# Performance work log

Measured on AMD Instinct MI355X. Metric: run time of the kernel, lower is better.

Reference implementation:

```python
import jax, jax.numpy as jnp
import numpy as np

B, S, F, D, U, DS = 128, 64, 32, 128, 128, 128  # batch, seq, features, feat_dim, units, static_dim
DIN = S * F * D + DS  # grn_concat input dim
EPS = 1e-3  # keras LayerNormalization default epsilon


def _ln(x, gamma, beta):
    m = jnp.mean(x, axis=-1, keepdims=True)
    v = jnp.mean(jnp.square(x - m), axis=-1, keepdims=True)
    return (x - m) * jax.lax.rsqrt(v + EPS) * gamma + beta


def setup_inputs() -> dict:
    key = jax.random.key(0)
    ks = iter(jax.random.split(key, 32))
    p = lambda *shape: jax.random.normal(next(ks), shape, dtype=jnp.float32) * 0.02
    inp = {
        "inputs": jax.random.normal(next(ks), (B, S, F * D), dtype=jnp.float32),
        "static_input": jax.random.normal(next(ks), (B, DS), dtype=jnp.float32),
        # grn_concat (input dim DIN != U -> project path active)
        "cWe": p(DIN, U), "cbe": jnp.zeros((U,), jnp.float32),
        "cWl": p(U, U), "cbl": jnp.zeros((U,), jnp.float32),
        "cWgl": p(U, U), "cbgl": jnp.zeros((U,), jnp.float32),
        "cWgs": p(U, U), "cbgs": jnp.zeros((U,), jnp.float32),
        "cgamma": jnp.ones((U,), jnp.float32), "cbeta": jnp.zeros((U,), jnp.float32),
        "cWp": p(DIN, U), "cbp": jnp.zeros((U,), jnp.float32),
        # softmax Dense: units -> num_features
        "Ws": p(U, F), "bs": jnp.zeros((F,), jnp.float32),
        # per-feature GRNs, stacked over feature axis (feat_dim == units -> no project)
        "fWe": p(F, D, U), "fbe": jnp.zeros((F, U), jnp.float32),
        "fWl": p(F, U, U), "fbl": jnp.zeros((F, U), jnp.float32),
        "fWgl": p(F, U, U), "fbgl": jnp.zeros((F, U), jnp.float32),
        "fWgs": p(F, U, U), "fbgs": jnp.zeros((F, U), jnp.float32),
        "fgamma": jnp.ones((F, U), jnp.float32), "fbeta": jnp.zeros((F, U), jnp.float32),
    }
    return inp


def reference(inputs, static_input, cWe, cbe, cWl, cbl, cWgl, cbgl, cWgs, cbgs,
              cgamma, cbeta, cWp, cbp, Ws, bs, fWe, fbe, fWl, fbl, fWgl, fbgl,
              fWgs, fbgs, fgamma, fbeta):
    b = inputs.shape[0]
    # --- selection weights: flatten + concat static, grn_concat, softmax dense ---
    v = jnp.concatenate([inputs.reshape(b, -1), static_input], axis=-1)  # [B, DIN]
    h = jax.nn.elu(v @ cWe + cbe)
    h = h @ cWl + cbl
    res = v @ cWp + cbp  # project (DIN != U)
    g = (h @ cWgl + cbgl) * jax.nn.sigmoid(h @ cWgs + cbgs)  # GLU
    y = _ln(res + g, cgamma, cbeta)  # [B, U]
    w = jax.nn.softmax(y @ Ws + bs, axis=-1)  # [B, F]
    # --- per-feature GRNs, batched over feature axis ---
    x = inputs.reshape(b, S, F, D)  # tf.split along axis 2
    h = jax.nn.elu(jnp.einsum('bsfd,fdu->bsfu', x, fWe) + fbe)
    h = jnp.einsum('bsfu,fuv->bsfv', h, fWl) + fbl
    g = (jnp.einsum('bsfu,fuv->bsfv', h, fWgl) + fbgl) * \
        jax.nn.sigmoid(jnp.einsum('bsfu,fuv->bsfv', h, fWgs) + fbgs)
    xg = _ln(x + g, fgamma, fbeta)  # [B, S, F, U]
    # --- softmax-weighted combine (v repeated over seq, matmul transpose_a) ---
    out = jnp.einsum('bf,bsfu->bsu', w, xg)  # [B, S, U]
    return out
```

## Files before the change

### kernel.cpp

```cpp
#include <hip/hip_runtime.h>


typedef unsigned short u16;
typedef __attribute__((ext_vector_type(4))) u16 u16x4;
typedef __attribute__((ext_vector_type(8))) u16 u16x8;
typedef __attribute__((ext_vector_type(8))) __bf16 bf16x8;
typedef __attribute__((ext_vector_type(4))) float f32x4;

__device__ __forceinline__ u16 f2bf(float f) {
  unsigned int x = __float_as_uint(f);
  return (u16)((x + 0x7fffu + ((x >> 16) & 1u)) >> 16);
}
__device__ __forceinline__ float eluf(float x) { return x > 0.f ? x : __expf(x) - 1.f; }
__device__ __forceinline__ float sigmoidf_(float x) { return 1.f / (1.f + __expf(-x)); }

#define MFMA_BF16(a, b, c) __builtin_amdgcn_mfma_f32_16x16x32_bf16((a), (b), (c), 0, 0, 0)

__global__ __launch_bounds__(512) void k0_prep(
    const float* __restrict__ fWe, const float* __restrict__ fWl,
    const float* __restrict__ fWgl, const float* __restrict__ fWgs,
    u16* __restrict__ wT)
{
  const int b = blockIdx.x, f = b >> 2, mat = b & 3;
  const float* srcs[4] = {fWe, fWl, fWgl, fWgs};
  const float* src = srcs[mat] + (size_t)f * 16384;
  u16* dst = wT + (size_t)b * 16384;
  const int n = threadIdx.x & 127, qc = threadIdx.x >> 7;
  for (int k8 = qc * 4; k8 < qc * 4 + 4; ++k8) {
    u16x8 p;
#pragma unroll
    for (int j = 0; j < 8; ++j) p[j] = f2bf(src[(k8 * 8 + j) * 128 + n]);
    *(u16x8*)&dst[n * 128 + k8 * 8] = p;
  }
}

__global__ __launch_bounds__(1024) void k1_bigmm(
    const float* __restrict__ inp, const float* __restrict__ cWe,
    const float* __restrict__ cWp, float* __restrict__ outE, float* __restrict__ outP)
{
  __shared__ __align__(16) u16 xA[2][128][64];
  __shared__ __align__(16) u16 wE[2][128][64];
  __shared__ __align__(16) u16 wP[2][128][64];
  const int t = threadIdx.x;
  const int lane = t & 63, wv = t >> 6, quad = lane >> 4, l16 = lane & 15;
  const int mat = wv >> 3, wvm = wv & 7;
  const int arow = t >> 3, af = t & 7;
  const int aslot = (af ^ (arow & 7)) * 8;
  const int wt = t & 511, wmi = t >> 9;
  const int wn = wt & 127, wkg = wt >> 7;
  const int wphi = (wn ^ (wn >> 2)) & 7;
  const float* Wm = wmi ? cWp : cWe;

  f32x4 acc[8];
#pragma unroll
  for (int n = 0; n < 8; ++n)
#pragma unroll
    for (int r = 0; r < 4; ++r) acc[n][r] = 0.f;

  const size_t kbase = (size_t)blockIdx.x * 1024;

  float4 av0[2], av1[2];
  float wv0[16], wv1[16];

  auto load_regs = [&](int it, float4* av, float* wr) {
    const size_t kk = kbase + (size_t)it * 64;
    av[0] = *(const float4*)(inp + (size_t)arow * 262144 + kk + af * 8);
    av[1] = *(const float4*)(inp + (size_t)arow * 262144 + kk + af * 8 + 4);
#pragma unroll
    for (int j = 0; j < 16; ++j)
      wr[j] = Wm[(kk + (size_t)(wkg * 16 + j)) * 128 + wn];
  };
  auto store_lds = [&](int buf, const float4* av, const float* wr) {
    u16x8 pa;
    pa[0] = f2bf(av[0].x); pa[1] = f2bf(av[0].y);
    pa[2] = f2bf(av[0].z); pa[3] = f2bf(av[0].w);
    pa[4] = f2bf(av[1].x); pa[5] = f2bf(av[1].y);
    pa[6] = f2bf(av[1].z); pa[7] = f2bf(av[1].w);
    *(u16x8*)&xA[buf][arow][aslot] = pa;
    u16 (*Wl)[64] = wmi ? wP[buf] : wE[buf];
#pragma unroll
    for (int s = 0; s < 2; ++s) {
      u16x8 pw;
#pragma unroll
      for (int j = 0; j < 8; ++j) pw[j] = f2bf(wr[s * 8 + j]);
      *(u16x8*)&Wl[wn][((wkg * 2 + s) ^ wphi) * 8] = pw;
    }
  };

  load_regs(0, av0, wv0);
  load_regs(1, av1, wv1);
  store_lds(0, av0, wv0);

  const int m = 16 * wvm + l16;
  const int phA = l16 & 7;
  const int phB = (l16 & 7) ^ (l16 >> 2);

  for (int it = 0; it < 16; ++it) {
    const int buf = it & 1;
    asm volatile("s_waitcnt lgkmcnt(0)" ::: "memory");
    __builtin_amdgcn_s_barrier();
    if (it < 14) {
      if (buf == 0) load_regs(it + 2, av0, wv0);
      else          load_regs(it + 2, av1, wv1);
    }
    const u16 (*Xb)[64] = xA[buf];
    const u16 (*WbT)[64] = mat ? wP[buf] : wE[buf];
#pragma unroll
    for (int ks = 0; ks < 2; ++ks) {
      const int slot = ks * 4 + quad;
      const bf16x8 a = *(const bf16x8*)&Xb[m][(slot ^ phA) * 8];
#pragma unroll
      for (int nt = 0; nt < 8; ++nt) {
        const bf16x8 b = *(const bf16x8*)&WbT[nt * 16 + l16][(slot ^ phB ^ ((nt & 1) * 4)) * 8];
        acc[nt] = MFMA_BF16(a, b, acc[nt]);
      }
    }
    if (it < 15) {
      if (buf == 0) store_lds(1, av1, wv1);
      else          store_lds(0, av0, wv0);
    }
  }
  float* outp = mat ? outP : outE;
#pragma unroll
  for (int nt = 0; nt < 8; ++nt) {
    const int col = nt * 16 + l16;
#pragma unroll
    for (int r = 0; r < 4; ++r) {
      const int row = 16 * wvm + quad * 4 + r;
      atomicAdd(&outp[row * 128 + col], acc[nt][r]);
    }
  }
}

__global__ __launch_bounds__(512) void k1b_small(
    const float* __restrict__ stat,
    const float* __restrict__ cWe, const float* __restrict__ cbe,
    const float* __restrict__ cWl, const float* __restrict__ cbl,
    const float* __restrict__ cWgl, const float* __restrict__ cbgl,
    const float* __restrict__ cWgs, const float* __restrict__ cbgs,
    const float* __restrict__ cgam, const float* __restrict__ cbet,
    const float* __restrict__ cWp, const float* __restrict__ cbp,
    const float* __restrict__ Ws, const float* __restrict__ bs,
    const float* __restrict__ preE, const float* __restrict__ preP,
    float* __restrict__ wout)
{
  const int b = blockIdx.x, t = threadIdx.x;
  const int u = t & 127, dc = t >> 7;
  __shared__ float shS[128], shA[128], shB[128], par[8][132], red[4];
  if (t < 128) shS[t] = stat[b * 128 + t];
  __syncthreads();

  const float* we = cWe + (size_t)262144 * 128;
  const float* wp = cWp + (size_t)262144 * 128;
  float hp = 0.f, rp = 0.f;
  for (int d = dc * 32; d < dc * 32 + 32; ++d) {
    const float sv = shS[d];
    hp += sv * we[d * 128 + u];
    rp += sv * wp[d * 128 + u];
  }
  par[dc][u] = hp; par[4 + dc][u] = rp;
  __syncthreads();

  float rs = 0.f;
  if (t < 128) {
    const float he = preE[b * 128 + t] + cbe[t] + par[0][t] + par[1][t] + par[2][t] + par[3][t];
    rs = preP[b * 128 + t] + cbp[t] + par[4][t] + par[5][t] + par[6][t] + par[7][t];
    shA[t] = eluf(he);
  }
  __syncthreads();

  float p = 0.f;
  for (int d = dc * 32; d < dc * 32 + 32; ++d) p += shA[d] * cWl[d * 128 + u];
  par[dc][u] = p;
  __syncthreads();
  if (t < 128) shB[t] = cbl[t] + par[0][t] + par[1][t] + par[2][t] + par[3][t];
  __syncthreads();

  float gp = 0.f, sp = 0.f;
  for (int d = dc * 32; d < dc * 32 + 32; ++d) {
    const float hv = shB[d];
    gp += hv * cWgl[d * 128 + u];
    sp += hv * cWgs[d * 128 + u];
  }
  par[dc][u] = gp; par[4 + dc][u] = sp;
  __syncthreads();

  float z = 0.f;
  if (t < 128) {
    const float gl = cbgl[t] + par[0][t] + par[1][t] + par[2][t] + par[3][t];
    const float gs = cbgs[t] + par[4][t] + par[5][t] + par[6][t] + par[7][t];
    z = rs + gl * sigmoidf_(gs);
  }
  float s = z, q = z * z;
#pragma unroll
  for (int off = 32; off >= 1; off >>= 1) { s += __shfl_xor(s, off); q += __shfl_xor(q, off); }
  if ((t & 63) == 0 && t < 128) { red[(t >> 6) * 2] = s; red[(t >> 6) * 2 + 1] = q; }
  __syncthreads();
  if (t < 128) {
    const float S = red[0] + red[2], Q = red[1] + red[3];
    const float mean = S * (1.f / 128.f);
    const float var = Q * (1.f / 128.f) - mean * mean;
    const float rstd = rsqrtf(var + 1e-3f);
    shA[t] = (z - mean) * rstd * cgam[t] + cbet[t];
  }
  __syncthreads();
  if (t < 32) {
    float sj = bs[t];
    for (int uu = 0; uu < 128; ++uu) sj += shA[uu] * Ws[uu * 32 + t];
    float m = sj;
#pragma unroll
    for (int off = 16; off >= 1; off >>= 1) m = fmaxf(m, __shfl_xor(m, off));
    const float e = __expf(sj - m);
    float se = e;
#pragma unroll
    for (int off = 16; off >= 1; off >>= 1) se += __shfl_xor(se, off);
    wout[b * 32 + t] = e / se;
  }
}

__device__ __forceinline__ void mm_half(const u16 A[][136], const u16 WT[][72],
                                        int wv, int quad, int l16, int kh, f32x4 acc[8])
{
#pragma unroll
  for (int ks = 0; ks < 2; ++ks) {
    const int kol = ks * 32 + quad * 8;
    const bf16x8 a = *(const bf16x8*)&A[16 * wv + l16][kh + kol];
#pragma unroll
    for (int nt = 0; nt < 8; ++nt) {
      const bf16x8 b = *(const bf16x8*)&WT[nt * 16 + l16][kol];
      acc[nt] = MFMA_BF16(a, b, acc[nt]);
    }
  }
}

__global__ __launch_bounds__(256) void k2_grn(
    const float* __restrict__ inp, const u16* __restrict__ wT,
    const float* __restrict__ fbe, const float* __restrict__ fbl,
    const float* __restrict__ fbgl, const float* __restrict__ fbgs,
    const float* __restrict__ fgam, const float* __restrict__ fbet,
    const float* __restrict__ wsel, float* __restrict__ out)
{
  __shared__ __align__(16) u16 xA[64][136];
  __shared__ __align__(16) u16 hA[64][136];
  __shared__ __align__(16) u16 WT[2][128][72];
  const int t = threadIdx.x;
  const int lane = t & 63, wv = t >> 6, quad = lane >> 4, l16 = lane & 15;
  const int bb = blockIdx.x & 127, fg = blockIdx.x >> 7;

  f32x4 acc[8], glr[8], racc[8];
#pragma unroll
  for (int n = 0; n < 8; ++n)
#pragma unroll
    for (int r = 0; r < 4; ++r) racc[n][r] = 0.f;

#define ZERO_ACC() do { _Pragma("unroll") \
  for (int n_ = 0; n_ < 8; ++n_) { acc[n_][0]=0.f; acc[n_][1]=0.f; acc[n_][2]=0.f; acc[n_][3]=0.f; } } while (0)

  u16x8 wreg[4];
  auto wt_load = [&](const u16* src) {
#pragma unroll
    for (int i = 0; i < 4; ++i) {
      const int u = t + i * 256;
      wreg[i] = *(const u16x8*)(src + (u >> 3) * 128 + (u & 7) * 8);
    }
  };
  auto wt_write = [&](int nb) {
#pragma unroll
    for (int i = 0; i < 4; ++i) {
      const int u = t + i * 256;
      *(u16x8*)&WT[nb][u >> 3][(u & 7) * 8] = wreg[i];
    }
  };

  for (int fi = 0; fi < 8; ++fi) {
    const int f = fg * 8 + fi;
    const float wb = wsel[bb * 32 + f];
    const u16* wf = wT + (size_t)f * 65536;

    __syncthreads();
#pragma unroll
    for (int i = 0; i < 8; ++i) {
      const int u = t + i * 256;
      const int row = u >> 5, fo = u & 31;
      const float4 v = *(const float4*)(inp + (size_t)(bb * 64 + row) * 4096 + f * 128 + fo * 4);
      u16x4 p; p[0] = f2bf(v.x); p[1] = f2bf(v.y); p[2] = f2bf(v.z); p[3] = f2bf(v.w);
      *(u16x4*)&xA[row][fo * 4] = p;
    }
    wt_load(wf);
    wt_write(0);
    __syncthreads();

    wt_load(wf + 64);
    ZERO_ACC();
    mm_half(xA, WT[0], wv, quad, l16, 0, acc);
    wt_write(1);
    __syncthreads();
    wt_load(wf + 16384);
    mm_half(xA, WT[1], wv, quad, l16, 64, acc);
#pragma unroll
    for (int nt = 0; nt < 8; ++nt) {
      const int col = nt * 16 + l16;
      const float bv = fbe[f * 128 + col];
#pragma unroll
      for (int r = 0; r < 4; ++r)
        hA[16 * wv + quad * 4 + r][col] = f2bf(eluf(acc[nt][r] + bv));
    }
    wt_write(0);
    __syncthreads();

    wt_load(wf + 16384 + 64);
    ZERO_ACC();
    mm_half(hA, WT[0], wv, quad, l16, 0, acc);
    wt_write(1);
    __syncthreads();
    wt_load(wf + 2 * 16384);
    mm_half(hA, WT[1], wv, quad, l16, 64, acc);
#pragma unroll
    for (int nt = 0; nt < 8; ++nt) {
      const int col = nt * 16 + l16;
      const float bv = fbl[f * 128 + col];
#pragma unroll
      for (int r = 0; r < 4; ++r)
        hA[16 * wv + quad * 4 + r][col] = f2bf(acc[nt][r] + bv);
    }
    wt_write(0);
    __syncthreads();

    wt_load(wf + 2 * 16384 + 64);
    ZERO_ACC();
    mm_half(hA, WT[0], wv, quad, l16, 0, acc);
    wt_write(1);
    __syncthreads();
    wt_load(wf + 3 * 16384);
    mm_half(hA, WT[1], wv, quad, l16, 64, acc);
#pragma unroll
    for (int nt = 0; nt < 8; ++nt) {
      const float bv = fbgl[f * 128 + nt * 16 + l16];
#pragma unroll
      for (int r = 0; r < 4; ++r) glr[nt][r] = acc[nt][r] + bv;
    }
    wt_write(0);
    __syncthreads();

    wt_load(wf + 3 * 16384 + 64);
    ZERO_ACC();
    mm_half(hA, WT[0], wv, quad, l16, 0, acc);
    wt_write(1);
    __syncthreads();
    mm_half(hA, WT[1], wv, quad, l16, 64, acc);

#pragma unroll
    for (int nt = 0; nt < 8; ++nt) {
      const int col = nt * 16 + l16;
      const float bv = fbgs[f * 128 + col];
#pragma unroll
      for (int r = 0; r < 4; ++r) {
        const float g = glr[nt][r] * sigmoidf_(acc[nt][r] + bv);
        const float x = __uint_as_float(((unsigned int)xA[16 * wv + quad * 4 + r][col]) << 16);
        acc[nt][r] = x + g;
      }
    }
    float sm[4], sq[4];
#pragma unroll
    for (int r = 0; r < 4; ++r) {
      float s = 0.f, q = 0.f;
#pragma unroll
      for (int nt = 0; nt < 8; ++nt) { const float zz = acc[nt][r]; s += zz; q += zz * zz; }
      sm[r] = s; sq[r] = q;
    }
#pragma unroll
    for (int off = 1; off <= 8; off <<= 1)
#pragma unroll
      for (int r = 0; r < 4; ++r) { sm[r] += __shfl_xor(sm[r], off); sq[r] += __shfl_xor(sq[r], off); }
#pragma unroll
    for (int r = 0; r < 4; ++r) {
      const float mean = sm[r] * (1.f / 128.f);
      const float var = sq[r] * (1.f / 128.f) - mean * mean;
      const float rstd = rsqrtf(var + 1e-3f);
      sm[r] = mean; sq[r] = rstd;
    }
#pragma unroll
    for (int nt = 0; nt < 8; ++nt) {
      const int col = nt * 16 + l16;
      const float gam = fgam[f * 128 + col];
      const float bet = fbet[f * 128 + col];
#pragma unroll
      for (int r = 0; r < 4; ++r) {
        const float xg = (acc[nt][r] - sm[r]) * sq[r] * gam + bet;
        racc[nt][r] += wb * xg;
      }
    }
  }

#pragma unroll
  for (int nt = 0; nt < 8; ++nt) {
    const int col = nt * 16 + l16;
#pragma unroll
    for (int r = 0; r < 4; ++r) {
      const int grow = bb * 64 + 16 * wv + quad * 4 + r;
      atomicAdd(&out[(size_t)grow * 128 + col], racc[nt][r]);
    }
  }
#undef ZERO_ACC
}

extern "C" void kernel_launch(void* const* d_in, const int* in_sizes, int n_in,
                              void* d_out, int out_size, void* d_ws, size_t ws_size,
                              hipStream_t stream)
{
  const float* inp    = (const float*)d_in[0];
  const float* stat   = (const float*)d_in[1];
  const float* cWe    = (const float*)d_in[2];
  const float* cbe    = (const float*)d_in[3];
  const float* cWl    = (const float*)d_in[4];
  const float* cbl    = (const float*)d_in[5];
  const float* cWgl   = (const float*)d_in[6];
  const float* cbgl   = (const float*)d_in[7];
  const float* cWgs   = (const float*)d_in[8];
  const float* cbgs   = (const float*)d_in[9];
  const float* cgamma = (const float*)d_in[10];
  const float* cbeta  = (const float*)d_in[11];
  const float* cWp    = (const float*)d_in[12];
  const float* cbp    = (const float*)d_in[13];
  const float* Ws     = (const float*)d_in[14];
  const float* bs     = (const float*)d_in[15];
  const float* fWe    = (const float*)d_in[16];
  const float* fbe    = (const float*)d_in[17];
  const float* fWl    = (const float*)d_in[18];
  const float* fbl    = (const float*)d_in[19];
  const float* fWgl   = (const float*)d_in[20];
  const float* fbgl   = (const float*)d_in[21];
  const float* fWgs   = (const float*)d_in[22];
  const float* fbgs   = (const float*)d_in[23];
  const float* fgam   = (const float*)d_in[24];
  const float* fbet   = (const float*)d_in[25];

  float* ws_he  = (float*)d_ws;
  float* ws_res = ws_he + 16384;
  float* ws_w   = ws_res + 16384;
  u16*   ws_wT  = (u16*)(ws_w + 4096);

  hipMemsetAsync(d_ws, 0, 32768 * sizeof(float), stream);
  hipMemsetAsync(d_out, 0, (size_t)out_size * sizeof(float), stream);
  k0_prep<<<128, 512, 0, stream>>>(fWe, fWl, fWgl, fWgs, ws_wT);
  k1_bigmm<<<256, 1024, 0, stream>>>(inp, cWe, cWp, ws_he, ws_res);
  k1b_small<<<128, 512, 0, stream>>>(stat, cWe, cbe, cWl, cbl, cWgl, cbgl, cWgs, cbgs,
                                     cgamma, cbeta, cWp, cbp, Ws, bs, ws_he, ws_res, ws_w);
  k2_grn<<<512, 256, 0, stream>>>(inp, ws_wT, fbe, fbl, fbgl, fbgs,
                                  fgam, fbet, ws_w, (float*)d_out);
}
```

Measured before the change: 592.3 us.

## Read GRN weights directly from global memory and drop shared-memory staging and barriers

The per-feature GRN kernel no longer stages transposed weight tiles through a double-buffered LDS buffer. Each wave now loads its MFMA B operands straight from global memory (expected to be L2-resident) and works only on its own 16 rows, so all block-level barriers go away. The grid doubles to 1024 blocks with each handling 4 features instead of 8, the block index order is changed so blocks sharing a batch row run adjacently, and launch bounds request 4 blocks per CU. The cost is that every wave re-reads the full weights from cache instead of sharing one LDS copy, and each output element receives twice as many atomic adds.

```diff
diff --git a/kernel.cpp b/kernel.cpp
--- a/kernel.cpp
+++ b/kernel.cpp
@@ -218,22 +218,7 @@
   }
 }
 
-__device__ __forceinline__ void mm_half(const u16 A[][136], const u16 WT[][72],
-                                        int wv, int quad, int l16, int kh, f32x4 acc[8])
-{
-#pragma unroll
-  for (int ks = 0; ks < 2; ++ks) {
-    const int kol = ks * 32 + quad * 8;
-    const bf16x8 a = *(const bf16x8*)&A[16 * wv + l16][kh + kol];
-#pragma unroll
-    for (int nt = 0; nt < 8; ++nt) {
-      const bf16x8 b = *(const bf16x8*)&WT[nt * 16 + l16][kol];
-      acc[nt] = MFMA_BF16(a, b, acc[nt]);
-    }
-  }
-}
-
-__global__ __launch_bounds__(256) void k2_grn(
+__global__ __launch_bounds__(256, 4) void k2_grn(
     const float* __restrict__ inp, const u16* __restrict__ wT,
     const float* __restrict__ fbe, const float* __restrict__ fbl,
     const float* __restrict__ fbgl, const float* __restrict__ fbgs,
@@ -242,10 +227,10 @@
 {
   __shared__ __align__(16) u16 xA[64][136];
   __shared__ __align__(16) u16 hA[64][136];
-  __shared__ __align__(16) u16 WT[2][128][72];
   const int t = threadIdx.x;
   const int lane = t & 63, wv = t >> 6, quad = lane >> 4, l16 = lane & 15;
-  const int bb = blockIdx.x & 127, fg = blockIdx.x >> 7;
+  const int fg = blockIdx.x & 7, bb = blockIdx.x >> 3;
+  const int rbase = wv * 16;
 
   f32x4 acc[8], glr[8], racc[8];
 #pragma unroll
@@ -256,98 +241,67 @@
 #define ZERO_ACC() do { _Pragma("unroll") \
   for (int n_ = 0; n_ < 8; ++n_) { acc[n_][0]=0.f; acc[n_][1]=0.f; acc[n_][2]=0.f; acc[n_][3]=0.f; } } while (0)
 
-  u16x8 wreg[4];
-  auto wt_load = [&](const u16* src) {
-#pragma unroll
-    for (int i = 0; i < 4; ++i) {
-      const int u = t + i * 256;
-      wreg[i] = *(const u16x8*)(src + (u >> 3) * 128 + (u & 7) * 8);
+  auto mm_g = [&](const u16 (*A)[136], const u16* __restrict__ wg, f32x4* ac) {
+#pragma unroll
+    for (int s = 0; s < 4; ++s) {
+      const int kol = s * 32 + quad * 8;
+      const bf16x8 a = *(const bf16x8*)&A[rbase + l16][kol];
+#pragma unroll
+      for (int nt = 0; nt < 8; ++nt) {
+        const bf16x8 b = *(const bf16x8*)(wg + (size_t)(nt * 16 + l16) * 128 + kol);
+        ac[nt] = MFMA_BF16(a, b, ac[nt]);
+      }
     }
   };
-  auto wt_write = [&](int nb) {
-#pragma unroll
-    for (int i = 0; i < 4; ++i) {
-      const int u = t + i * 256;
-      *(u16x8*)&WT[nb][u >> 3][(u & 7) * 8] = wreg[i];
-    }
-  };
-
-  for (int fi = 0; fi < 8; ++fi) {
-    const int f = fg * 8 + fi;
+
+  for (int fi = 0; fi < 4; ++fi) {
+    const int f = fg * 4 + fi;
     const float wb = wsel[bb * 32 + f];
     const u16* wf = wT + (size_t)f * 65536;
 
-    __syncthreads();
+    const float* xsrc = inp + (size_t)(bb * 64 + rbase) * 4096 + f * 128;
 #pragma unroll
     for (int i = 0; i < 8; ++i) {
-      const int u = t + i * 256;
-      const int row = u >> 5, fo = u & 31;
-      const float4 v = *(const float4*)(inp + (size_t)(bb * 64 + row) * 4096 + f * 128 + fo * 4);
+      const int idx = i * 64 + lane;
+      const int row = idx >> 5, fo = idx & 31;
+      const float4 v = *(const float4*)(xsrc + (size_t)row * 4096 + fo * 4);
       u16x4 p; p[0] = f2bf(v.x); p[1] = f2bf(v.y); p[2] = f2bf(v.z); p[3] = f2bf(v.w);
-      *(u16x4*)&xA[row][fo * 4] = p;
-    }
-    wt_load(wf);
-    wt_write(0);
-    __syncthreads();
-
-    wt_load(wf + 64);
+      *(u16x4*)&xA[rbase + row][fo * 4] = p;
+    }
+
     ZERO_ACC();
-    mm_half(xA, WT[0], wv, quad, l16, 0, acc);
-    wt_write(1);
-    __syncthreads();
-    wt_load(wf + 16384);
-    mm_half(xA, WT[1], wv, quad, l16, 64, acc);
+    mm_g(xA, wf, acc);
 #pragma unroll
     for (int nt = 0; nt < 8; ++nt) {
       const int col = nt * 16 + l16;
       const float bv = fbe[f * 128 + col];
 #pragma unroll
       for (int r = 0; r < 4; ++r)
-        hA[16 * wv + quad * 4 + r][col] = f2bf(eluf(acc[nt][r] + bv));
-    }
-    wt_write(0);
-    __syncthreads();
-
-    wt_load(wf + 16384 + 64);
+        hA[rbase + quad * 4 + r][col] = f2bf(eluf(acc[nt][r] + bv));
+    }
+
     ZERO_ACC();
-    mm_half(hA, WT[0], wv, quad, l16, 0, acc);
-    wt_write(1);
-    __syncthreads();
-    wt_load(wf + 2 * 16384);
-    mm_half(hA, WT[1], wv, quad, l16, 64, acc);
+    mm_g(hA, wf + 16384, acc);
 #pragma unroll
     for (int nt = 0; nt < 8; ++nt) {
       const int col = nt * 16 + l16;
       const float bv = fbl[f * 128 + col];
 #pragma unroll
       for (int r = 0; r < 4; ++r)
-        hA[16 * wv + quad * 4 + r][col] = f2bf(acc[nt][r] + bv);
-    }
-    wt_write(0);
-    __syncthreads();
-
-    wt_load(wf + 2 * 16384 + 64);
+        hA[rbase + quad * 4 + r][col] = f2bf(acc[nt][r] + bv);
+    }
+
     ZERO_ACC();
-    mm_half(hA, WT[0], wv, quad, l16, 0, acc);
-    wt_write(1);
-    __syncthreads();
-    wt_load(wf + 3 * 16384);
-    mm_half(hA, WT[1], wv, quad, l16, 64, acc);
+    mm_g(hA, wf + 2 * 16384, acc);
 #pragma unroll
     for (int nt = 0; nt < 8; ++nt) {
       const float bv = fbgl[f * 128 + nt * 16 + l16];
 #pragma unroll
       for (int r = 0; r < 4; ++r) glr[nt][r] = acc[nt][r] + bv;
     }
-    wt_write(0);
-    __syncthreads();
-
-    wt_load(wf + 3 * 16384 + 64);
+
     ZERO_ACC();
-    mm_half(hA, WT[0], wv, quad, l16, 0, acc);
-    wt_write(1);
-    __syncthreads();
-    mm_half(hA, WT[1], wv, quad, l16, 64, acc);
+    mm_g(hA, wf + 3 * 16384, acc);
 
 #pragma unroll
     for (int nt = 0; nt < 8; ++nt) {
@@ -356,7 +310,7 @@
 #pragma unroll
       for (int r = 0; r < 4; ++r) {
         const float g = glr[nt][r] * sigmoidf_(acc[nt][r] + bv);
-        const float x = __uint_as_float(((unsigned int)xA[16 * wv + quad * 4 + r][col]) << 16);
+        const float x = __uint_as_float(((unsigned int)xA[rbase + quad * 4 + r][col]) << 16);
         acc[nt][r] = x + g;
       }
     }
@@ -397,7 +351,7 @@
     const int col = nt * 16 + l16;
 #pragma unroll
     for (int r = 0; r < 4; ++r) {
-      const int grow = bb * 64 + 16 * wv + quad * 4 + r;
+      const int grow = bb * 64 + rbase + quad * 4 + r;
       atomicAdd(&out[(size_t)grow * 128 + col], racc[nt][r]);
     }
   }
@@ -446,6 +400,6 @@
   k1_bigmm<<<256, 1024, 0, stream>>>(inp, cWe, cWp, ws_he, ws_res);
   k1b_small<<<128, 512, 0, stream>>>(stat, cWe, cbe, cWl, cbl, cWgl, cbgl, cWgs, cbgs,
                                      cgamma, cbeta, cWp, cbp, Ws, bs, ws_he, ws_res, ws_w);
-  k2_grn<<<512, 256, 0, stream>>>(inp, ws_wT, fbe, fbl, fbgl, fbgs,
-                                  fgam, fbet, ws_w, (float*)d_out);
-}
+  k2_grn<<<1024, 256, 0, stream>>>(inp, ws_wT, fbe, fbl, fbgl, fbgs,
+                                   fgam, fbet, ws_w, (float*)d_out);
+}
```

After: 765.4 us. +29.2%, slower.
